# Kernel tuning notes

Hardware: AMD Instinct MI355X
Metric: run time of the kernel (lower is better)

Reference implementation:

```python
import jax, jax.numpy as jnp
import numpy as np

D = 2048
H = 16
HD = D // H
B = 2
T = 2048
EPS = 1e-5


def _gated(x, W, b, Wg, bg):
    # MoEGatedLinear: linear output elementwise-gated by sigmoid of a linear router
    return (x @ W.T + b) * jax.nn.sigmoid(x @ Wg.T + bg)


def _ln(x, g, b):
    m = jnp.mean(x, axis=-1, keepdims=True)
    v = jnp.mean((x - m) ** 2, axis=-1, keepdims=True)
    return (x - m) * jax.lax.rsqrt(v + EPS) * g + b


def setup_inputs() -> dict:
    key = jax.random.key(0)
    ks = jax.random.split(key, 16)
    w = lambda k, o, i: (jax.random.normal(k, (o, i), jnp.float32) * 0.02)
    inp = {"x": jax.random.normal(ks[0], (B, T, D), jnp.float32)}
    for i, n in enumerate(["q", "k", "v", "o"]):
        inp[f"W_{n}"] = w(jax.random.fold_in(ks[1], i), D, D)
        inp[f"b_{n}"] = jnp.zeros((D,), jnp.float32)
        inp[f"Wg_{n}"] = w(jax.random.fold_in(ks[2], i), D, D)
        inp[f"bg_{n}"] = jnp.zeros((D,), jnp.float32)
    inp["W_in"] = w(ks[3], 4 * D, D)
    inp["b_in"] = jnp.zeros((4 * D,), jnp.float32)
    inp["Wg_in"] = w(ks[4], 4 * D, D)
    inp["bg_in"] = jnp.zeros((4 * D,), jnp.float32)
    inp["W_out"] = w(ks[5], D, 4 * D)
    inp["b_out"] = jnp.zeros((D,), jnp.float32)
    inp["Wg_out"] = w(ks[6], D, 4 * D)
    inp["bg_out"] = jnp.zeros((D,), jnp.float32)
    inp["ln1_g"] = jnp.ones((D,), jnp.float32)
    inp["ln1_b"] = jnp.zeros((D,), jnp.float32)
    inp["ln2_g"] = jnp.ones((D,), jnp.float32)
    inp["ln2_b"] = jnp.zeros((D,), jnp.float32)
    return inp


def reference(x, W_q, b_q, Wg_q, bg_q, W_k, b_k, Wg_k, bg_k, W_v, b_v, Wg_v, bg_v,
              W_o, b_o, Wg_o, bg_o, W_in, b_in, Wg_in, bg_in, W_out, b_out, Wg_out, bg_out,
              ln1_g, ln1_b, ln2_g, ln2_b):
    Bb, Tt, C = x.shape
    resid = x
    h = _ln(x, ln1_g, ln1_b)
    q = _gated(h, W_q, b_q, Wg_q, bg_q).reshape(Bb, Tt, H, HD).transpose(0, 2, 1, 3)
    k = _gated(h, W_k, b_k, Wg_k, bg_k).reshape(Bb, Tt, H, HD).transpose(0, 2, 1, 3)
    v = _gated(h, W_v, b_v, Wg_v, bg_v).reshape(Bb, Tt, H, HD).transpose(0, 2, 1, 3)
    att = jnp.einsum('bhqd,bhkd->bhqk', q, k) * (1.0 / np.sqrt(HD))
    att = jax.nn.softmax(att, axis=-1)  # full (no causal mask) per source
    y = jnp.einsum('bhqk,bhkd->bhqd', att, v)
    y = y.transpose(0, 2, 1, 3).reshape(Bb, Tt, C)
    y = _gated(y, W_o, b_o, Wg_o, bg_o)
    x = resid + y
    resid = x
    h = _ln(x, ln2_g, ln2_b)
    h = _gated(h, W_in, b_in, Wg_in, bg_in)
    h = jax.nn.gelu(h, approximate=False)  # torch nn.GELU default = exact erf
    h = _gated(h, W_out, b_out, Wg_out, bg_out)
    return resid + h
```

## Files before the change

### kernel.cpp

```cpp
#include <hip/hip_runtime.h>
#include <cstdint>
#include <cmath>

#define DD 2048
#define TT 2048
#define HH 16
#define HDD 128
#define MROWS 4096

typedef __attribute__((ext_vector_type(8))) short s16x8;
typedef __attribute__((ext_vector_type(4))) float f32x4;

typedef const __attribute__((address_space(1))) void gvoid;
typedef __attribute__((address_space(3))) void lvoid;

__device__ __forceinline__ void async_cp16(const void* g, void* l) {
    __builtin_amdgcn_global_load_lds((gvoid*)g, (lvoid*)l, 16, 0, 0);
}

__device__ __forceinline__ unsigned short f2bf(float f) {
    unsigned int u = __float_as_uint(f);
    u += 0x7fffu + ((u >> 16) & 1u);
    return (unsigned short)(u >> 16);
}

__device__ __forceinline__ void store4bf(unsigned short* p, float a, float b, float c, float d) {
    union { unsigned short u[4]; uint2 v; } x;
    x.u[0] = f2bf(a); x.u[1] = f2bf(b); x.u[2] = f2bf(c); x.u[3] = f2bf(d);
    *(uint2*)p = x.v;
}

__global__ __launch_bounds__(256) void cvt_ilv(const float* __restrict__ W,
                                               const float* __restrict__ Wg,
                                               unsigned short* __restrict__ out, int k4shift) {
    int g = blockIdx.x * 256 + threadIdx.x;
    int rp = g >> k4shift;
    int c4 = g & ((1 << k4shift) - 1);
    int jb = rp >> 5, s = rp & 15, sel = (rp >> 4) & 1;
    const float* src = (sel ? Wg : W) + (((size_t)(jb * 16 + s)) << (k4shift + 2)) + c4 * 4;
    float4 v = *(const float4*)src;
    store4bf(out + (((size_t)rp) << (k4shift + 2)) + c4 * 4, v.x, v.y, v.z, v.w);
}

__global__ __launch_bounds__(256) void ln_bf16(const float* __restrict__ x,
                                               const float* __restrict__ gg,
                                               const float* __restrict__ bb,
                                               unsigned short* __restrict__ out) {
    __shared__ float red[8];
    const int row = blockIdx.x, t = threadIdx.x;
    const float* xr = x + (size_t)row * DD;
    float4 a = ((const float4*)xr)[t];
    float4 c = ((const float4*)xr)[t + 256];
    float s = a.x + a.y + a.z + a.w + c.x + c.y + c.z + c.w;
    float q = a.x*a.x + a.y*a.y + a.z*a.z + a.w*a.w + c.x*c.x + c.y*c.y + c.z*c.z + c.w*c.w;
    #pragma unroll
    for (int m = 1; m < 64; m <<= 1) { s += __shfl_xor(s, m); q += __shfl_xor(q, m); }
    if ((t & 63) == 0) { red[t >> 6] = s; red[4 + (t >> 6)] = q; }
    __syncthreads();
    s = red[0] + red[1] + red[2] + red[3];
    q = red[4] + red[5] + red[6] + red[7];
    float mean = s * (1.f / DD);
    float var = q * (1.f / DD) - mean * mean;
    float rstd = rsqrtf(var + 1e-5f);
    float4 g1 = ((const float4*)gg)[t], b1 = ((const float4*)bb)[t];
    float4 g2 = ((const float4*)gg)[t + 256], b2 = ((const float4*)bb)[t + 256];
    unsigned short* orow = out + (size_t)row * DD;
    store4bf(orow + 4 * t,
             (a.x - mean) * rstd * g1.x + b1.x, (a.y - mean) * rstd * g1.y + b1.y,
             (a.z - mean) * rstd * g1.z + b1.z, (a.w - mean) * rstd * g1.w + b1.w);
    store4bf(orow + 1024 + 4 * t,
             (c.x - mean) * rstd * g2.x + b2.x, (c.y - mean) * rstd * g2.y + b2.y,
             (c.z - mean) * rstd * g2.z + b2.z, (c.w - mean) * rstd * g2.w + b2.w);
}

#define G8_LDA(base, iq) do { \
    _Pragma("unroll") \
    for (int i2_ = 0; i2_ < 4; i2_++) \
        af[i2_] = *(const s16x8*)(lds + (base) + aRd + ((iq) * 4 + i2_) * 1024); \
} while (0)
#define G8_LDB(base) do { \
    _Pragma("unroll") \
    for (int j_ = 0; j_ < 4; j_++) \
        bf[j_] = *(const s16x8*)(lds + (base) + bRd + j_ * 1024); \
} while (0)
#define G8_MMA(iq) do { \
    __builtin_amdgcn_s_setprio(1); \
    _Pragma("unroll") \
    for (int i2_ = 0; i2_ < 4; i2_++) { \
        _Pragma("unroll") \
        for (int j_ = 0; j_ < 4; j_++) \
            acc[(iq) * 4 + i2_][j_] = __builtin_amdgcn_mfma_f32_16x16x32_bf16( \
                af[i2_], bf[j_], acc[(iq) * 4 + i2_][j_], 0, 0, 0); \
    } \
    __builtin_amdgcn_s_setprio(0); \
} while (0)
#define G8_BAR() __builtin_amdgcn_s_barrier()
#define G8_SCB() __builtin_amdgcn_sched_barrier(0)
#define G8_VM4() asm volatile("s_waitcnt vmcnt(4)" ::: "memory")
#define G8_VM0() asm volatile("s_waitcnt vmcnt(0)" ::: "memory")

template <int EPI>
__global__ __launch_bounds__(512, 2) void gemm_gated8(
        const unsigned short* __restrict__ A, const unsigned short* __restrict__ Wi,
        const float* __restrict__ bias, const float* __restrict__ biasg,
        const float* __restrict__ resid, void* __restrict__ outp,
        int M, int Ntrue, int K) {
    __shared__ unsigned short lds_[65536];
    char* lds = (char*)lds_;
    const int t = threadIdx.x, lane = t & 63, wv = t >> 6;
    const int fr = lane & 15, fg = lane >> 4;
    const int wr = wv >> 2, wc = wv & 3;

    const int nM = M >> 8;
    const int nwg = gridDim.x;
    const int pid = blockIdx.x;
    const int swz = (pid & 7) * (nwg >> 3) + (pid >> 3);
    const int nt = swz / nM;
    const int mt = swz - nt * nM;
    const int m0 = mt << 8;
    const int np0 = nt << 8;

    const unsigned short* aP[2];
    const unsigned short* bP[2];
    int ldst[2];
    #pragma unroll
    for (int l = 0; l < 2; l++) {
        int idx = l * 512 + t;
        int p = idx >> 3, pc = idx & 7;
        int spc = pc ^ (p & 7);
        int lr = 2 * p + (spc >> 2);
        int ke = (spc & 3) * 8;
        aP[l] = A + (size_t)(m0 + lr) * K + ke;
        bP[l] = Wi + (size_t)(np0 + lr) * K + ke;
        ldst[l] = idx * 16;
    }
    const int chR = (((fr & 1) << 2) | fg) ^ ((fr >> 1) & 7);
    const int aRd = (wr * 64 + (fr >> 1)) * 128 + chR * 16;
    const int bRd = (wc * 32 + (fr >> 1)) * 128 + chR * 16;

    f32x4 acc[8][4];
    f32x4 zero4 = {0.f, 0.f, 0.f, 0.f};
    #pragma unroll
    for (int i = 0; i < 8; i++)
        #pragma unroll
        for (int j = 0; j < 4; j++) acc[i][j] = zero4;
    s16x8 af[4], bf[4];

    async_cp16(aP[0], lds + ldst[0]);
    async_cp16(aP[1], lds + ldst[1]);
    async_cp16(bP[0], lds + 65536 + ldst[0]);
    async_cp16(bP[1], lds + 65536 + ldst[1]);
    async_cp16(aP[0] + 32, lds + 16384 + ldst[0]);
    async_cp16(aP[1] + 32, lds + 16384 + ldst[1]);
    async_cp16(bP[0] + 32, lds + 65536 + 16384 + ldst[0]);
    async_cp16(bP[1] + 32, lds + 65536 + 16384 + ldst[1]);
    G8_VM4(); G8_BAR(); G8_SCB();

    const int NT = K >> 6;
    for (int kt = 0; kt < NT - 1; kt++) {
        const int sA = (kt & 1) << 15;
        const int sB = 65536 + sA;
        const int nAb = sA ^ 32768;
        const int nBb = 65536 + nAb;
        const int kn = (kt + 1) << 6;
        G8_LDA(sA, 0); G8_LDB(sB);
        async_cp16(aP[0] + kn, lds + nAb + ldst[0]);
        async_cp16(aP[1] + kn, lds + nAb + ldst[1]);
        G8_MMA(0);
        G8_LDA(sA, 1);
        async_cp16(bP[0] + kn, lds + nBb + ldst[0]);
        async_cp16(bP[1] + kn, lds + nBb + ldst[1]);
        G8_MMA(1);
        G8_VM4(); G8_BAR(); G8_SCB();
        G8_LDA(sA + 16384, 0); G8_LDB(sB + 16384);
        async_cp16(aP[0] + kn + 32, lds + nAb + 16384 + ldst[0]);
        async_cp16(aP[1] + kn + 32, lds + nAb + 16384 + ldst[1]);
        G8_MMA(0);
        G8_LDA(sA + 16384, 1);
        async_cp16(bP[0] + kn + 32, lds + nBb + 16384 + ldst[0]);
        async_cp16(bP[1] + kn + 32, lds + nBb + 16384 + ldst[1]);
        G8_MMA(1);
        G8_VM4(); G8_BAR(); G8_SCB();
    }
    {
        const int sA = ((NT - 1) & 1) << 15;
        const int sB = 65536 + sA;
        G8_LDA(sA, 0); G8_LDB(sB);
        G8_MMA(0);
        G8_LDA(sA, 1);
        G8_MMA(1);
        G8_VM0(); G8_BAR(); G8_SCB();
        G8_LDA(sA + 16384, 0); G8_LDB(sB + 16384);
        G8_MMA(0);
        G8_LDA(sA + 16384, 1);
        G8_MMA(1);
    }

    const int mB = m0 + wr * 128 + fg * 4;
    const int nB = (nt << 7) + wc * 32 + fr;
    if constexpr (EPI == 1) {
        const int b_ = m0 >> 11;
        unsigned short* vt = (unsigned short*)outp;
        #pragma unroll
        for (int i = 0; i < 8; i++)
            #pragma unroll
            for (int jp = 0; jp < 2; jp++) {
                const int n = nB + jp * 16;
                const float bn = bias[n], bgn = biasg[n];
                float g4[4];
                #pragma unroll
                for (int r = 0; r < 4; r++) {
                    float lin = acc[i][2 * jp][r] + bn;
                    float gt = acc[i][2 * jp + 1][r] + bgn;
                    g4[r] = lin / (1.f + __expf(-gt));
                }
                unsigned short* dst = vt + ((size_t)b_ * 2048 + n) * 2048 +
                                      (m0 & 2047) + wr * 128 + i * 16 + fg * 4;
                store4bf(dst, g4[0], g4[1], g4[2], g4[3]);
            }
    } else {
        #pragma unroll
        for (int i = 0; i < 8; i++)
            #pragma unroll
            for (int jp = 0; jp < 2; jp++) {
                const int n = nB + jp * 16;
                const float bn = bias[n], bgn = biasg[n];
                #pragma unroll
                for (int r = 0; r < 4; r++) {
                    const int m = mB + i * 16 + r;
                    float lin = acc[i][2 * jp][r] + bn;
                    float gt = acc[i][2 * jp + 1][r] + bgn;
                    float gv = lin / (1.f + __expf(-gt));
                    if constexpr (EPI == 0) {
                        ((unsigned short*)outp)[(size_t)m * Ntrue + n] = f2bf(gv);
                    } else if constexpr (EPI == 2) {
                        ((float*)outp)[(size_t)m * Ntrue + n] =
                            resid[(size_t)m * Ntrue + n] + gv;
                    } else {
                        float ge = 0.5f * gv * (1.f + erff(gv * 0.70710678118f));
                        ((unsigned short*)outp)[(size_t)m * Ntrue + n] = f2bf(ge);
                    }
                }
            }
    }
}

__global__ __launch_bounds__(256, 4) void attn_flash2(const unsigned short* __restrict__ Q,
                                                      const unsigned short* __restrict__ Kb,
                                                      const unsigned short* __restrict__ VT,
                                                      unsigned short* __restrict__ Y) {
    __shared__ unsigned short sK[64 * 128];
    __shared__ unsigned short sV[128 * 64];
    __shared__ unsigned short sP[4 * 1024];
    const int t = threadIdx.x, lane = t & 63, wv = t >> 6;
    const int bx = blockIdx.x;
    const int qblk = bx & 31;
    const int h = (bx >> 5) & 15;
    const int b = bx >> 9;
    const int q0 = qblk * 64 + wv * 16;
    const int fr = lane & 15, fg = lane >> 4;

    s16x8 qf[4];
    const unsigned short* qbase = Q + ((size_t)(b * TT + q0 + fr)) * DD + h * HDD + fg * 8;
    #pragma unroll
    for (int s = 0; s < 4; s++) qf[s] = *(const s16x8*)(qbase + s * 32);

    const unsigned short* kSrc[4];
    const unsigned short* vSrc[4];
    #pragma unroll
    for (int r = 0; r < 4; r++) {
        int R = r * 16 + (t >> 4);
        int c = (t & 15) ^ ((t >> 4) & 15);
        kSrc[r] = Kb + (size_t)(b * TT + R) * DD + h * HDD + c * 8;
        int hd = r * 32 + (t >> 3);
        int cv = (t & 7) ^ ((t >> 3) & 7);
        vSrc[r] = VT + ((size_t)((b * HH + h) * HDD + hd)) * TT + cv * 8;
    }
    unsigned short* sPw = sP + wv * 1024;

    f32x4 zero4 = {0.f, 0.f, 0.f, 0.f};
    f32x4 o[8];
    #pragma unroll
    for (int jo = 0; jo < 8; jo++) o[jo] = zero4;
    float Mx[4], L[4];
    #pragma unroll
    for (int r = 0; r < 4; r++) { Mx[r] = -1e30f; L[r] = 0.f; }
    const float scale = 0.08838834764831845f;

    for (int tk0 = 0; tk0 < TT; tk0 += 64) {
        #pragma unroll
        for (int r = 0; r < 4; r++) {
            async_cp16(kSrc[r] + (size_t)tk0 * DD, sK + r * 2048 + t * 8);
            async_cp16(vSrc[r] + tk0, sV + r * 2048 + t * 8);
        }
        __syncthreads();

        f32x4 sac[4];
        #pragma unroll
        for (int j = 0; j < 4; j++) sac[j] = zero4;
        #pragma unroll
        for (int j = 0; j < 4; j++)
            #pragma unroll
            for (int s = 0; s < 4; s++) {
                s16x8 kf = *(const s16x8*)(sK + (j * 16 + fr) * 128 + (((s * 4 + fg) ^ fr) * 8));
                sac[j] = __builtin_amdgcn_mfma_f32_16x16x32_bf16(qf[s], kf, sac[j], 0, 0, 0);
            }

        float alpha[4];
        #pragma unroll
        for (int j = 0; j < 4; j++)
            #pragma unroll
            for (int r = 0; r < 4; r++) sac[j][r] *= scale;
        #pragma unroll
        for (int r = 0; r < 4; r++) {
            float mx = fmaxf(fmaxf(sac[0][r], sac[1][r]), fmaxf(sac[2][r], sac[3][r]));
            mx = fmaxf(mx, __shfl_xor(mx, 1));
            mx = fmaxf(mx, __shfl_xor(mx, 2));
            mx = fmaxf(mx, __shfl_xor(mx, 4));
            mx = fmaxf(mx, __shfl_xor(mx, 8));
            float mnew = fmaxf(Mx[r], mx);
            alpha[r] = __expf(Mx[r] - mnew);
            Mx[r] = mnew;
        }
        float rs[4] = {0.f, 0.f, 0.f, 0.f};
        #pragma unroll
        for (int j = 0; j < 4; j++)
            #pragma unroll
            for (int r = 0; r < 4; r++) {
                float p = __expf(sac[j][r] - Mx[r]);
                rs[r] += p;
                int qr = fg * 4 + r;
                int cc = (j * 2 + (fr >> 3)) ^ (qr & 7);
                sPw[qr * 64 + cc * 8 + (fr & 7)] = f2bf(p);
            }
        #pragma unroll
        for (int r = 0; r < 4; r++) {
            float tsum = rs[r];
            tsum += __shfl_xor(tsum, 1);
            tsum += __shfl_xor(tsum, 2);
            tsum += __shfl_xor(tsum, 4);
            tsum += __shfl_xor(tsum, 8);
            L[r] = L[r] * alpha[r] + tsum;
        }
        #pragma unroll
        for (int jo = 0; jo < 8; jo++)
            #pragma unroll
            for (int r = 0; r < 4; r++) o[jo][r] *= alpha[r];

        s16x8 pa[2];
        #pragma unroll
        for (int ks = 0; ks < 2; ks++)
            pa[ks] = *(const s16x8*)(sPw + fr * 64 + (((ks * 4 + fg) ^ (fr & 7)) * 8));
        #pragma unroll
        for (int jo = 0; jo < 8; jo++)
            #pragma unroll
            for (int ks = 0; ks < 2; ks++) {
                s16x8 vf = *(const s16x8*)(sV + (jo * 16 + fr) * 64 + (((ks * 4 + fg) ^ (fr & 7)) * 8));
                o[jo] = __builtin_amdgcn_mfma_f32_16x16x32_bf16(pa[ks], vf, o[jo], 0, 0, 0);
            }
        __syncthreads();
    }
    float Linv[4];
    #pragma unroll
    for (int r = 0; r < 4; r++) Linv[r] = 1.f / L[r];
    #pragma unroll
    for (int jo = 0; jo < 8; jo++)
        #pragma unroll
        for (int r = 0; r < 4; r++) {
            float val = o[jo][r] * Linv[r];
            Y[((size_t)(b * TT + q0 + fg * 4 + r)) * DD + h * HDD + jo * 16 + fr] = f2bf(val);
        }
}

extern "C" void kernel_launch(void* const* d_in, const int* in_sizes, int n_in,
                              void* d_out, int out_size, void* d_ws, size_t ws_size,
                              hipStream_t stream) {
    const float* x = (const float*)d_in[0];
    auto F = [&](int i) { return (const float*)d_in[i]; };
    char* ws = (char*)d_ws;
    const size_t MB = 1ull << 20;

    unsigned short* wi_q  = (unsigned short*)(ws + 0 * MB);
    unsigned short* wi_k  = (unsigned short*)(ws + 16 * MB);
    unsigned short* wi_v  = (unsigned short*)(ws + 32 * MB);
    unsigned short* wi_o  = (unsigned short*)(ws + 48 * MB);
    unsigned short* wi_in = (unsigned short*)(ws + 64 * MB);
    unsigned short* wi_ot = (unsigned short*)(ws + 128 * MB);
    cvt_ilv<<<dim3(8192), dim3(256), 0, stream>>>(F(1), F(3), wi_q, 9);
    cvt_ilv<<<dim3(8192), dim3(256), 0, stream>>>(F(5), F(7), wi_k, 9);
    cvt_ilv<<<dim3(8192), dim3(256), 0, stream>>>(F(9), F(11), wi_v, 9);
    cvt_ilv<<<dim3(8192), dim3(256), 0, stream>>>(F(13), F(15), wi_o, 9);
    cvt_ilv<<<dim3(32768), dim3(256), 0, stream>>>(F(17), F(19), wi_in, 9);
    cvt_ilv<<<dim3(32768), dim3(256), 0, stream>>>(F(21), F(23), wi_ot, 11);

    unsigned short* hbf = (unsigned short*)(ws + 192 * MB);
    unsigned short* qb  = (unsigned short*)(ws + 208 * MB);
    unsigned short* kb  = (unsigned short*)(ws + 224 * MB);
    unsigned short* vtb = (unsigned short*)(ws + 240 * MB);
    unsigned short* yb  = (unsigned short*)(ws + 256 * MB);
    unsigned short* ub  = (unsigned short*)(ws + 208 * MB);
    float* x1 = (float*)(ws + 272 * MB);

    ln_bf16<<<dim3(MROWS), dim3(256), 0, stream>>>(x, F(25), F(26), hbf);

    dim3 blk(512);
    gemm_gated8<0><<<dim3(256), blk, 0, stream>>>(hbf, wi_q, F(2), F(4), nullptr, qb, MROWS, DD, DD);
    gemm_gated8<0><<<dim3(256), blk, 0, stream>>>(hbf, wi_k, F(6), F(8), nullptr, kb, MROWS, DD, DD);
    gemm_gated8<1><<<dim3(256), blk, 0, stream>>>(hbf, wi_v, F(10), F(12), nullptr, vtb, MROWS, DD, DD);

    attn_flash2<<<dim3(1024), dim3(256), 0, stream>>>(qb, kb, vtb, yb);

    gemm_gated8<2><<<dim3(256), blk, 0, stream>>>(yb, wi_o, F(14), F(16), x, x1, MROWS, DD, DD);

    ln_bf16<<<dim3(MROWS), dim3(256), 0, stream>>>(x1, F(27), F(28), hbf);

    gemm_gated8<3><<<dim3(1024), blk, 0, stream>>>(hbf, wi_in, F(18), F(20), nullptr, ub, MROWS, 4 * DD, DD);
    gemm_gated8<2><<<dim3(256), blk, 0, stream>>>(ub, wi_ot, F(22), F(24), x1, (float*)d_out, MROWS, DD, 4 * DD);
}
```

Measured before the change: 1.370 ms.

## Load GEMM B operand directly from global into registers, halving LDS footprint

The gated GEMM stops staging the weight (B) tile through LDS. Each wave now loads its B fragments straight from global memory into a double-buffered register set, while only A stays in LDS. The wave layout changes from 2x4 to 4x2, so each wave computes 64x128 instead of 128x64. This removes the B LDS traffic and halves shared memory use. The costs are higher register pressure, redundant B global loads across waves, and uncoalesced strided row reads of the weights.

```diff
diff --git a/kernel.cpp b/kernel.cpp
--- a/kernel.cpp
+++ b/kernel.cpp
@@ -73,31 +73,31 @@
              (c.z - mean) * rstd * g2.z + b2.z, (c.w - mean) * rstd * g2.w + b2.w);
 }
 
-#define G8_LDA(base, iq) do { \
+#define G8_LDA(base) do { \
     _Pragma("unroll") \
-    for (int i2_ = 0; i2_ < 4; i2_++) \
-        af[i2_] = *(const s16x8*)(lds + (base) + aRd + ((iq) * 4 + i2_) * 1024); \
+    for (int i_ = 0; i_ < 4; i_++) \
+        af[i_] = *(const s16x8*)(lds + (base) + aRd + i_ * 1024); \
 } while (0)
-#define G8_LDB(base) do { \
+#define G8_BLOAD(dst, koff) do { \
     _Pragma("unroll") \
-    for (int j_ = 0; j_ < 4; j_++) \
-        bf[j_] = *(const s16x8*)(lds + (base) + bRd + j_ * 1024); \
+    for (int j_ = 0; j_ < 8; j_++) \
+        dst[j_] = *(const s16x8*)(bLane + (size_t)(j_ * 16) * K + (koff)); \
 } while (0)
-#define G8_MMA(iq) do { \
+#define G8_MMA(brx) do { \
     __builtin_amdgcn_s_setprio(1); \
     _Pragma("unroll") \
-    for (int i2_ = 0; i2_ < 4; i2_++) { \
+    for (int i_ = 0; i_ < 4; i_++) { \
         _Pragma("unroll") \
-        for (int j_ = 0; j_ < 4; j_++) \
-            acc[(iq) * 4 + i2_][j_] = __builtin_amdgcn_mfma_f32_16x16x32_bf16( \
-                af[i2_], bf[j_], acc[(iq) * 4 + i2_][j_], 0, 0, 0); \
+        for (int j_ = 0; j_ < 8; j_++) \
+            acc[i_][j_] = __builtin_amdgcn_mfma_f32_16x16x32_bf16( \
+                af[i_], brx[j_], acc[i_][j_], 0, 0, 0); \
     } \
     __builtin_amdgcn_s_setprio(0); \
 } while (0)
 #define G8_BAR() __builtin_amdgcn_s_barrier()
 #define G8_SCB() __builtin_amdgcn_sched_barrier(0)
-#define G8_VM4() asm volatile("s_waitcnt vmcnt(4)" ::: "memory")
-#define G8_VM0() asm volatile("s_waitcnt vmcnt(0)" ::: "memory")
+#define G8_VM16() asm volatile("s_waitcnt vmcnt(16)" ::: "memory")
+#define G8_VM8() asm volatile("s_waitcnt vmcnt(8)" ::: "memory")
 
 template <int EPI>
 __global__ __launch_bounds__(512, 2) void gemm_gated8(
@@ -105,11 +105,11 @@
         const float* __restrict__ bias, const float* __restrict__ biasg,
         const float* __restrict__ resid, void* __restrict__ outp,
         int M, int Ntrue, int K) {
-    __shared__ unsigned short lds_[65536];
+    __shared__ unsigned short lds_[32768];
     char* lds = (char*)lds_;
     const int t = threadIdx.x, lane = t & 63, wv = t >> 6;
     const int fr = lane & 15, fg = lane >> 4;
-    const int wr = wv >> 2, wc = wv & 3;
+    const int wr = wv >> 1, wc = wv & 1;
 
     const int nM = M >> 8;
     const int nwg = gridDim.x;
@@ -121,7 +121,6 @@
     const int np0 = nt << 8;
 
     const unsigned short* aP[2];
-    const unsigned short* bP[2];
     int ldst[2];
     #pragma unroll
     for (int l = 0; l < 2; l++) {
@@ -131,80 +130,64 @@
         int lr = 2 * p + (spc >> 2);
         int ke = (spc & 3) * 8;
         aP[l] = A + (size_t)(m0 + lr) * K + ke;
-        bP[l] = Wi + (size_t)(np0 + lr) * K + ke;
         ldst[l] = idx * 16;
     }
     const int chR = (((fr & 1) << 2) | fg) ^ ((fr >> 1) & 7);
-    const int aRd = (wr * 64 + (fr >> 1)) * 128 + chR * 16;
-    const int bRd = (wc * 32 + (fr >> 1)) * 128 + chR * 16;
-
-    f32x4 acc[8][4];
+    const int aRd = (wr * 32 + (fr >> 1)) * 128 + chR * 16;
+    const unsigned short* bLane = Wi + (size_t)(np0 + wc * 128 + fr) * K + fg * 8;
+
+    f32x4 acc[4][8];
     f32x4 zero4 = {0.f, 0.f, 0.f, 0.f};
     #pragma unroll
-    for (int i = 0; i < 8; i++)
-        #pragma unroll
-        for (int j = 0; j < 4; j++) acc[i][j] = zero4;
-    s16x8 af[4], bf[4];
-
+    for (int i = 0; i < 4; i++)
+        #pragma unroll
+        for (int j = 0; j < 8; j++) acc[i][j] = zero4;
+    s16x8 af[4], br0[8], br1[8];
+
+    G8_BLOAD(br0, 0);
     async_cp16(aP[0], lds + ldst[0]);
     async_cp16(aP[1], lds + ldst[1]);
-    async_cp16(bP[0], lds + 65536 + ldst[0]);
-    async_cp16(bP[1], lds + 65536 + ldst[1]);
     async_cp16(aP[0] + 32, lds + 16384 + ldst[0]);
     async_cp16(aP[1] + 32, lds + 16384 + ldst[1]);
-    async_cp16(bP[0] + 32, lds + 65536 + 16384 + ldst[0]);
-    async_cp16(bP[1] + 32, lds + 65536 + 16384 + ldst[1]);
-    G8_VM4(); G8_BAR(); G8_SCB();
+    G8_BLOAD(br1, 32);
+    G8_VM8();
+    G8_BAR(); G8_SCB();
 
     const int NT = K >> 6;
     for (int kt = 0; kt < NT - 1; kt++) {
         const int sA = (kt & 1) << 15;
-        const int sB = 65536 + sA;
         const int nAb = sA ^ 32768;
-        const int nBb = 65536 + nAb;
         const int kn = (kt + 1) << 6;
-        G8_LDA(sA, 0); G8_LDB(sB);
+        G8_LDA(sA);
         async_cp16(aP[0] + kn, lds + nAb + ldst[0]);
         async_cp16(aP[1] + kn, lds + nAb + ldst[1]);
-        G8_MMA(0);
-        G8_LDA(sA, 1);
-        async_cp16(bP[0] + kn, lds + nBb + ldst[0]);
-        async_cp16(bP[1] + kn, lds + nBb + ldst[1]);
-        G8_MMA(1);
-        G8_VM4(); G8_BAR(); G8_SCB();
-        G8_LDA(sA + 16384, 0); G8_LDB(sB + 16384);
         async_cp16(aP[0] + kn + 32, lds + nAb + 16384 + ldst[0]);
         async_cp16(aP[1] + kn + 32, lds + nAb + 16384 + ldst[1]);
-        G8_MMA(0);
-        G8_LDA(sA + 16384, 1);
-        async_cp16(bP[0] + kn + 32, lds + nBb + 16384 + ldst[0]);
-        async_cp16(bP[1] + kn + 32, lds + nBb + 16384 + ldst[1]);
-        G8_MMA(1);
-        G8_VM4(); G8_BAR(); G8_SCB();
+        G8_MMA(br0);
+        G8_BLOAD(br0, kn);
+        G8_LDA(sA + 16384);
+        G8_MMA(br1);
+        G8_BLOAD(br1, kn + 32);
+        G8_VM16();
+        G8_BAR(); G8_SCB();
     }
     {
         const int sA = ((NT - 1) & 1) << 15;
-        const int sB = 65536 + sA;
-        G8_LDA(sA, 0); G8_LDB(sB);
-        G8_MMA(0);
-        G8_LDA(sA, 1);
-        G8_MMA(1);
-        G8_VM0(); G8_BAR(); G8_SCB();
-        G8_LDA(sA + 16384, 0); G8_LDB(sB + 16384);
-        G8_MMA(0);
-        G8_LDA(sA + 16384, 1);
-        G8_MMA(1);
-    }
-
-    const int mB = m0 + wr * 128 + fg * 4;
-    const int nB = (nt << 7) + wc * 32 + fr;
+        G8_LDA(sA);
+        G8_MMA(br0);
+        G8_LDA(sA + 16384);
+        G8_MMA(br1);
+    }
+
+    const int mB = m0 + wr * 64 + fg * 4;
+    const int nB = (nt << 7) + wc * 64 + fr;
     if constexpr (EPI == 1) {
         const int b_ = m0 >> 11;
         unsigned short* vt = (unsigned short*)outp;
         #pragma unroll
-        for (int i = 0; i < 8; i++)
-            #pragma unroll
-            for (int jp = 0; jp < 2; jp++) {
+        for (int i = 0; i < 4; i++)
+            #pragma unroll
+            for (int jp = 0; jp < 4; jp++) {
                 const int n = nB + jp * 16;
                 const float bn = bias[n], bgn = biasg[n];
                 float g4[4];
@@ -215,14 +198,14 @@
                     g4[r] = lin / (1.f + __expf(-gt));
                 }
                 unsigned short* dst = vt + ((size_t)b_ * 2048 + n) * 2048 +
-                                      (m0 & 2047) + wr * 128 + i * 16 + fg * 4;
+                                      (m0 & 2047) + wr * 64 + i * 16 + fg * 4;
                 store4bf(dst, g4[0], g4[1], g4[2], g4[3]);
             }
     } else {
         #pragma unroll
-        for (int i = 0; i < 8; i++)
-            #pragma unroll
-            for (int jp = 0; jp < 2; jp++) {
+        for (int i = 0; i < 4; i++)
+            #pragma unroll
+            for (int jp = 0; jp < 4; jp++) {
                 const int n = nB + jp * 16;
                 const float bn = bias[n], bgn = biasg[n];
                 #pragma unroll
```

New measurement: 2.380 ms. +73.7%, slower.
